# Kernel tuning notes

Hardware: AMD Instinct MI355X
Metric: run time of the kernel (lower is better)

The kernel has to match this reference:

```python
import jax, jax.numpy as jnp
import numpy as np

B, T, HS, H, R = 4, 2048, 1024, 16, 16
D = HS // H  # 64 head_dim
LOGIT_01 = float(np.log(0.1 / 0.9))    # g_proj bias init
LOGIT_098 = float(np.log(0.98 / 0.02)) # base decay logits init


def _rope_cos_sin(seq_len, dim, base=10000.0):
    half = dim // 2
    inv_freq = 1.0 / (base ** (jnp.arange(half, dtype=jnp.float32) / half))
    freqs = jnp.arange(seq_len, dtype=jnp.float32)[:, None] * inv_freq[None, :]  # [T, half]
    return jnp.cos(freqs), jnp.sin(freqs)


def _apply_rope(x, cos, sin):
    # x: [B,T,H,D] with D even; rotate interleaved pairs over full D
    c = cos[None, :, None, :]
    s = sin[None, :, None, :]
    x1 = x[..., 0::2]
    x2 = x[..., 1::2]
    r1 = x1 * c - x2 * s
    r2 = x1 * s + x2 * c
    return jnp.stack((r1, r2), axis=-1).reshape(x.shape)


def setup_inputs() -> dict:
    key = jax.random.key(0)
    ks = jax.random.split(key, 10)
    def rn(k, shape, s=0.02):
        return jax.random.normal(k, shape, dtype=jnp.float32) * s
    return {
        "x": jax.random.normal(ks[0], (B, T, HS), dtype=jnp.float32),
        "q_w": rn(ks[1], (HS, HS)),
        "k_w": rn(ks[2], (HS, HS)),
        "v_w": rn(ks[3], (HS, HS)),
        "Wq": rn(ks[4], (H, R, D), 0.05),
        "Wk": rn(ks[5], (H, R, D), 0.05),
        "g_w": rn(ks[6], (H * R, HS)),
        "g_b": jnp.full((H * R,), LOGIT_01, dtype=jnp.float32),
        "base_decay_logits": jnp.full((H, R), LOGIT_098, dtype=jnp.float32),
        "out_w": rn(ks[7], (HS, HS)),
        "out_b": jnp.zeros((HS,), dtype=jnp.float32),
        "ln_g": jnp.ones((HS,), dtype=jnp.float32),
        "ln_b": jnp.zeros((HS,), dtype=jnp.float32),
    }


def reference(x, q_w, k_w, v_w, Wq, Wk, g_w, g_b, base_decay_logits,
              out_w, out_b, ln_g, ln_b):
    b, t, hs = x.shape
    h, r, d = Wq.shape
    # qkv projections (torch Linear: x @ W.T)
    q = (x @ q_w.T).reshape(b, t, h, d)
    k = (x @ k_w.T).reshape(b, t, h, d)
    v = (x @ v_w.T).reshape(b, t, h, d)
    # RoPE (dim_rot == head_dim since it is even)
    cos, sin = _rope_cos_sin(t, d)
    q = _apply_rope(q, cos, sin)
    k = _apply_rope(k, cos, sin)
    # low-rank projections
    q_r = jnp.einsum('bthd,hrd->bthr', q, Wq)
    k_r = jnp.einsum('bthd,hrd->bthr', k, Wk)
    # content gates
    g = jax.nn.sigmoid((x @ g_w.T + g_b).reshape(b, t, h, r))
    decay = jax.nn.sigmoid(base_decay_logits)[None, :, :, None]  # [1,H,r,1]
    scale = 1.0 / jnp.sqrt(jnp.asarray(d, dtype=x.dtype))

    def step(M, inp):
        q_t, k_t, v_t, g_t = inp  # [B,H,r], [B,H,r], [B,H,D], [B,H,r]
        M = M * decay + jnp.einsum('bhr,bhd->bhrd', g_t * k_t * scale, v_t)
        y = jnp.einsum('bhr,bhrd->bhd', q_t, M)
        return M, y

    xs = (q_r.transpose(1, 0, 2, 3), k_r.transpose(1, 0, 2, 3),
          v.transpose(1, 0, 2, 3), g.transpose(1, 0, 2, 3))
    M0 = jnp.zeros((b, h, r, d), dtype=x.dtype)
    _, Y = jax.lax.scan(step, M0, xs)  # Y: [T,B,H,D]
    Y = Y.transpose(1, 0, 2, 3).reshape(b, t, hs)
    out = Y @ out_w.T + out_b  # dropout is identity at eval time
    hres = x + out
    mu = jnp.mean(hres, axis=-1, keepdims=True)
    var = jnp.mean((hres - mu) ** 2, axis=-1, keepdims=True)
    return (hres - mu) / jnp.sqrt(var + 1e-5) * ln_g + ln_b
```

## Files before the change

kernel.cpp:

```cpp
#include <hip/hip_runtime.h>
#include <hip/hip_bf16.h>

#define B_ 4
#define T_ 2048
#define HS_ 1024
#define H_ 16
#define R_ 16
#define D_ 64
#define BT_ (B_*T_)
#define NC_ 3328
#define CHUNK_ 64
#define NCHUNK_ (T_/CHUNK_)

typedef __attribute__((ext_vector_type(8))) short short8;
typedef __attribute__((ext_vector_type(4))) float f32x4;

__device__ __forceinline__ float b2f(ushort u){
    union{unsigned int i; float f;} v; v.i = ((unsigned int)u) << 16; return v.f;
}
__device__ __forceinline__ ushort f2b(float f){
    __hip_bfloat16 h = __float2bfloat16(f);
    return *reinterpret_cast<ushort*>(&h);
}
__device__ __forceinline__ float sigm(float x){ return 1.f/(1.f+expf(-x)); }

__device__ __forceinline__ void gl_lds16(const void* g, void* l){
    __builtin_amdgcn_global_load_lds((const __attribute__((address_space(1))) void*)g,
                                     (__attribute__((address_space(3))) void*)l,
                                     16, 0, 0);
}

__global__ void k_cast4(const float* __restrict__ src, ushort* __restrict__ dst){
    int i = blockIdx.x*256 + threadIdx.x;
    float4 v = ((const float4*)src)[i];
    ushort4 o; o.x=f2b(v.x); o.y=f2b(v.y); o.z=f2b(v.z); o.w=f2b(v.w);
    ((ushort4*)dst)[i] = o;
}

__global__ void k_build_wcat(const float* __restrict__ qw, const float* __restrict__ kw,
                             const float* __restrict__ vw, const float* __restrict__ gw,
                             ushort* __restrict__ wcat){
    int i = blockIdx.x*256 + threadIdx.x;
    int e = i*4;
    int row = e >> 10, col = e & 1023;
    const float* src;
    if      (row < 1024) src = qw + (size_t)row*1024 + col;
    else if (row < 2048) src = kw + (size_t)(row-1024)*1024 + col;
    else if (row < 3072) src = vw + (size_t)(row-2048)*1024 + col;
    else                 src = gw + (size_t)(row-3072)*1024 + col;
    float4 v = *(const float4*)src;
    ushort4 o; o.x=f2b(v.x); o.y=f2b(v.y); o.z=f2b(v.z); o.w=f2b(v.w);
    ((ushort4*)wcat)[i] = o;
}

__global__ void k_rope_tab(float* __restrict__ cosT, float* __restrict__ sinT){
    int i = blockIdx.x*256 + threadIdx.x;
    int t = i >> 5, f = i & 31;
    float inv = powf(10000.f, -(float)f/32.f);
    float a = (float)t * inv;
    cosT[i] = cosf(a);
    sinT[i] = sinf(a);
}

__global__ __launch_bounds__(256) void k_gemm_bt(const ushort* __restrict__ A,
                                                 const ushort* __restrict__ Bm,
                                                 ushort* __restrict__ C,
                                                 int K, int ldc){
    __shared__ __align__(16) ushort Asl[128*32];
    __shared__ __align__(16) ushort Bsl[128*32];
    int tid  = threadIdx.x;
    int lane = tid & 63, wid = tid >> 6;
    int wrow = (wid >> 1)*64, wcol = (wid & 1)*64;
    long arow0 = (long)blockIdx.x * 128;
    long brow0 = (long)blockIdx.y * 128;

    int srow = tid >> 2, sseg = (tid & 3)*8;
    const ushort* ga0 = A  + (arow0      + srow)*(size_t)K + sseg;
    const ushort* ga1 = ga0 + 64*(size_t)K;
    const ushort* gb0 = Bm + (brow0      + srow)*(size_t)K + sseg;
    const ushort* gb1 = gb0 + 64*(size_t)K;
    ushort* la0 = &Asl[(tid>>6)*512];
    ushort* la1 = la0 + 2048;
    ushort* lb0 = &Bsl[(tid>>6)*512];
    ushort* lb1 = lb0 + 2048;

    f32x4 acc[4][4];
#pragma unroll
    for(int m=0;m<4;m++)
#pragma unroll
        for(int n=0;n<4;n++)
            acc[m][n] = (f32x4){0.f,0.f,0.f,0.f};

    int fr = lane & 15, fg = lane >> 4;
    for(int kt=0; kt<K; kt+=32){
        __syncthreads();
        gl_lds16(ga0 + kt, la0);
        gl_lds16(ga1 + kt, la1);
        gl_lds16(gb0 + kt, lb0);
        gl_lds16(gb1 + kt, lb1);
        __syncthreads();

        short8 af[4], bfr[4];
#pragma unroll
        for(int m=0;m<4;m++) af[m]  = *(const short8*)&Asl[(wrow + m*16 + fr)*32 + fg*8];
#pragma unroll
        for(int n=0;n<4;n++) bfr[n] = *(const short8*)&Bsl[(wcol + n*16 + fr)*32 + fg*8];
#pragma unroll
        for(int m=0;m<4;m++)
#pragma unroll
            for(int n=0;n<4;n++)
                acc[m][n] = __builtin_amdgcn_mfma_f32_16x16x32_bf16(af[m], bfr[n], acc[m][n], 0,0,0);
    }

#pragma unroll
    for(int m=0;m<4;m++)
#pragma unroll
        for(int n=0;n<4;n++){
            long col = brow0 + wcol + n*16 + fr;
#pragma unroll
            for(int j=0;j<4;j++){
                long row = arow0 + wrow + m*16 + fg*4 + j;
                C[row*(long)ldc + col] = f2b(acc[m][n][j]);
            }
        }
}

__global__ __launch_bounds__(256) void k_rope_proj(const ushort* __restrict__ qkvg,
                                                   const float* __restrict__ cosT,
                                                   const float* __restrict__ sinT,
                                                   const float* __restrict__ Wq,
                                                   const float* __restrict__ Wk,
                                                   const float* __restrict__ gb,
                                                   float* __restrict__ qr_s,
                                                   float* __restrict__ gk_s){
    __shared__ __align__(16) ushort lq[64*72], lk[64*72];
    __shared__ __align__(16) ushort wql[16*72], wkl[16*72];
    int tid = threadIdx.x, wid = tid >> 6, lane = tid & 63;
    int bt0 = blockIdx.x * 64;
    int h   = blockIdx.y;

    {
        int row = tid >> 4, seg = tid & 15;
        float4 wq4 = *(const float4*)(Wq + (size_t)h*1024 + row*64 + seg*4);
        float4 wk4 = *(const float4*)(Wk + (size_t)h*1024 + row*64 + seg*4);
        ushort* dq = &wql[row*72 + seg*4];
        ushort* dk = &wkl[row*72 + seg*4];
        dq[0]=f2b(wq4.x); dq[1]=f2b(wq4.y); dq[2]=f2b(wq4.z); dq[3]=f2b(wq4.w);
        dk[0]=f2b(wk4.x); dk[1]=f2b(wk4.y); dk[2]=f2b(wk4.z); dk[3]=f2b(wk4.w);
    }

#pragma unroll
    for(int rep=0; rep<2; ++rep){
        int flat = rep*256 + tid;
        int row = flat >> 3, seg = flat & 7;
        int t = (bt0 + row) & 2047;
        const ushort* base = qkvg + (size_t)(bt0+row)*NC_ + h*64 + seg*8;
        short8 q8 = *(const short8*)base;
        short8 k8 = *(const short8*)(base + 1024);
        float4 cv = *(const float4*)&cosT[t*32 + seg*4];
        float4 sv = *(const float4*)&sinT[t*32 + seg*4];
        float qf[8], kf[8];
#pragma unroll
        for(int j=0;j<8;j++){ qf[j]=b2f((ushort)q8[j]); kf[j]=b2f((ushort)k8[j]); }
        float c4[4] = {cv.x,cv.y,cv.z,cv.w};
        float s4[4] = {sv.x,sv.y,sv.z,sv.w};
        short8 qo, ko;
#pragma unroll
        for(int p=0;p<4;p++){
            float c=c4[p], s=s4[p];
            qo[2*p]   = (short)f2b(qf[2*p]*c - qf[2*p+1]*s);
            qo[2*p+1] = (short)f2b(qf[2*p]*s + qf[2*p+1]*c);
            ko[2*p]   = (short)f2b(kf[2*p]*c - kf[2*p+1]*s);
            ko[2*p+1] = (short)f2b(kf[2*p]*s + kf[2*p+1]*c);
        }
        *(short8*)&lq[row*72 + seg*8] = qo;
        *(short8*)&lk[row*72 + seg*8] = ko;
    }
    __syncthreads();

    int fr = lane & 15, fg = lane >> 4;
    int wrow = wid*16;
    short8 aq0 = *(const short8*)&lq[(wrow+fr)*72 + fg*8];
    short8 aq1 = *(const short8*)&lq[(wrow+fr)*72 + 32 + fg*8];
    short8 ak0 = *(const short8*)&lk[(wrow+fr)*72 + fg*8];
    short8 ak1 = *(const short8*)&lk[(wrow+fr)*72 + 32 + fg*8];
    short8 bq0 = *(const short8*)&wql[fr*72 + fg*8];
    short8 bq1 = *(const short8*)&wql[fr*72 + 32 + fg*8];
    short8 bk0 = *(const short8*)&wkl[fr*72 + fg*8];
    short8 bk1 = *(const short8*)&wkl[fr*72 + 32 + fg*8];
    f32x4 accq = (f32x4){0.f,0.f,0.f,0.f};
    f32x4 acck = (f32x4){0.f,0.f,0.f,0.f};
    accq = __builtin_amdgcn_mfma_f32_16x16x32_bf16(aq0, bq0, accq, 0,0,0);
    accq = __builtin_amdgcn_mfma_f32_16x16x32_bf16(aq1, bq1, accq, 0,0,0);
    acck = __builtin_amdgcn_mfma_f32_16x16x32_bf16(ak0, bk0, acck, 0,0,0);
    acck = __builtin_amdgcn_mfma_f32_16x16x32_bf16(ak1, bk1, acck, 0,0,0);

    int r = fr;
    float gbv = gb[h*16 + r];
#pragma unroll
    for(int j=0;j<4;j++){
        int bt = bt0 + wrow + fg*4 + j;
        int t  = bt & 2047, b = bt >> 11;
        size_t o = (((size_t)(b*16 + h))*2048 + t)*16 + r;
        qr_s[o] = accq[j];
        float gl = b2f(qkvg[(size_t)bt*NC_ + 3072 + h*16 + r]) + gbv;
        gk_s[o] = sigm(gl) * acck[j] * 0.125f;
    }
}

__global__ __launch_bounds__(64) void k_scan_local(const ushort* __restrict__ qkvg,
                                                   const float* __restrict__ gk_s,
                                                   const float* __restrict__ bdl,
                                                   float* __restrict__ Mloc){
    int lane = threadIdx.x;
    int bx = blockIdx.x;
    int ch = bx & (NCHUNK_-1), bh = bx >> 5;
    int b = bh >> 4, h = bh & 15;
    float dec[16], M[16];
#pragma unroll
    for(int r=0;r<16;r++){ dec[r] = sigm(bdl[h*16+r]); M[r] = 0.f; }

    int t0 = ch*CHUNK_;
    const float4*  gk4 = (const float4*)(gk_s + (((size_t)bh)*2048 + t0)*16);
    const ushort*  vp  = qkvg + ((size_t)(b*2048 + t0))*NC_ + 2048 + h*64 + lane;
    for(int tt=0; tt<CHUNK_; ++tt){
        float v = b2f(*vp); vp += NC_;
        float4 a0 = gk4[0], a1 = gk4[1], a2 = gk4[2], a3 = gk4[3]; gk4 += 4;
        float gk[16] = {a0.x,a0.y,a0.z,a0.w, a1.x,a1.y,a1.z,a1.w,
                        a2.x,a2.y,a2.z,a2.w, a3.x,a3.y,a3.z,a3.w};
#pragma unroll
        for(int r=0;r<16;r++) M[r] = fmaf(M[r], dec[r], gk[r]*v);
    }
    float* mp = Mloc + ((size_t)bx)*1024 + lane;
#pragma unroll
    for(int r=0;r<16;r++) mp[r*64] = M[r];
}

__global__ __launch_bounds__(64) void k_scan_carry(float* __restrict__ Mloc,
                                                   const float* __restrict__ bdl){
    int lane = threadIdx.x;
    int sub = blockIdx.x & 3, bh = blockIdx.x >> 2, h = bh & 15;
    float decC[4], S[4];
#pragma unroll
    for(int rr=0;rr<4;rr++){
        decC[rr] = powf(sigm(bdl[h*16 + sub*4 + rr]), (float)CHUNK_);
        S[rr] = 0.f;
    }
    for(int c=0;c<NCHUNK_;c++){
        float* p = Mloc + ((size_t)(bh*NCHUNK_ + c))*1024 + lane + sub*4*64;
#pragma unroll
        for(int rr=0;rr<4;rr++){
            float m = p[rr*64];
            p[rr*64] = S[rr];
            S[rr] = fmaf(S[rr], decC[rr], m);
        }
    }
}

__global__ __launch_bounds__(64) void k_scan_out(const ushort* __restrict__ qkvg,
                                                 const float* __restrict__ gk_s,
                                                 const float* __restrict__ qr_s,
                                                 const float* __restrict__ Mst,
                                                 const float* __restrict__ bdl,
                                                 ushort* __restrict__ Ybf){
    int lane = threadIdx.x;
    int bx = blockIdx.x;
    int ch = bx & (NCHUNK_-1), bh = bx >> 5;
    int b = bh >> 4, h = bh & 15;
    float dec[16], M[16];
#pragma unroll
    for(int r=0;r<16;r++) dec[r] = sigm(bdl[h*16+r]);
    const float* sp = Mst + ((size_t)bx)*1024 + lane;
#pragma unroll
    for(int r=0;r<16;r++) M[r] = sp[r*64];

    int t0 = ch*CHUNK_;
    const float4* gk4 = (const float4*)(gk_s + (((size_t)bh)*2048 + t0)*16);
    const float4* q4  = (const float4*)(qr_s + (((size_t)bh)*2048 + t0)*16);
    const ushort* vp  = qkvg + ((size_t)(b*2048 + t0))*NC_ + 2048 + h*64 + lane;
    ushort*       yp  = Ybf  + ((size_t)(b*2048 + t0))*1024 + h*64 + lane;
    for(int tt=0; tt<CHUNK_; ++tt){
        float v = b2f(*vp); vp += NC_;
        float4 a0 = gk4[0], a1 = gk4[1], a2 = gk4[2], a3 = gk4[3]; gk4 += 4;
        float4 b0 = q4[0],  b1 = q4[1],  b2 = q4[2],  b3 = q4[3];  q4  += 4;
        float gk[16] = {a0.x,a0.y,a0.z,a0.w, a1.x,a1.y,a1.z,a1.w,
                        a2.x,a2.y,a2.z,a2.w, a3.x,a3.y,a3.z,a3.w};
        float qv[16] = {b0.x,b0.y,b0.z,b0.w, b1.x,b1.y,b1.z,b1.w,
                        b2.x,b2.y,b2.z,b2.w, b3.x,b3.y,b3.z,b3.w};
        float y = 0.f;
#pragma unroll
        for(int r=0;r<16;r++){
            M[r] = fmaf(M[r], dec[r], gk[r]*v);
            y    = fmaf(qv[r], M[r], y);
        }
        *yp = f2b(y); yp += 1024;
    }
}

__global__ __launch_bounds__(256) void k_ln(const float* __restrict__ x,
                                            const ushort* __restrict__ O,
                                            const float* __restrict__ ob,
                                            const float* __restrict__ lg,
                                            const float* __restrict__ lb,
                                            float* __restrict__ out){
    __shared__ float red[8];
    int row = blockIdx.x, tid = threadIdx.x;
    float hv[4];
    float sum = 0.f, ssq = 0.f;
#pragma unroll
    for(int k2=0;k2<4;k2++){
        int j = tid + k2*256;
        float v = x[(size_t)row*1024 + j] + b2f(O[(size_t)row*1024 + j]) + ob[j];
        hv[k2] = v; sum += v; ssq += v*v;
    }
#pragma unroll
    for(int off=32; off; off >>= 1){
        sum += __shfl_down(sum, off, 64);
        ssq += __shfl_down(ssq, off, 64);
    }
    int wid = tid >> 6, lane = tid & 63;
    if(lane == 0){ red[wid] = sum; red[4+wid] = ssq; }
    __syncthreads();
    if(tid == 0){
        float s = red[0]+red[1]+red[2]+red[3];
        float q = red[4]+red[5]+red[6]+red[7];
        float mu = s / 1024.f;
        red[0] = mu;
        red[1] = q / 1024.f - mu*mu;
    }
    __syncthreads();
    float mu = red[0];
    float inv = rsqrtf(red[1] + 1e-5f);
#pragma unroll
    for(int k2=0;k2<4;k2++){
        int j = tid + k2*256;
        out[(size_t)row*1024 + j] = (hv[k2]-mu)*inv*lg[j] + lb[j];
    }
}

extern "C" void kernel_launch(void* const* d_in, const int* in_sizes, int n_in,
                              void* d_out, int out_size, void* d_ws, size_t ws_size,
                              hipStream_t stream){
    const float* x    = (const float*)d_in[0];
    const float* q_w  = (const float*)d_in[1];
    const float* k_w  = (const float*)d_in[2];
    const float* v_w  = (const float*)d_in[3];
    const float* Wq   = (const float*)d_in[4];
    const float* Wk   = (const float*)d_in[5];
    const float* g_w  = (const float*)d_in[6];
    const float* g_b  = (const float*)d_in[7];
    const float* bdl  = (const float*)d_in[8];
    const float* outw = (const float*)d_in[9];
    const float* outb = (const float*)d_in[10];
    const float* ln_g = (const float*)d_in[11];
    const float* ln_b = (const float*)d_in[12];
    float* out = (float*)d_out;

    char* ws = (char*)d_ws;
    size_t off = 0;
    ushort* xbf  = (ushort*)(ws + off); off += (size_t)BT_*HS_*2;
    ushort* wcat = (ushort*)(ws + off); off += (size_t)NC_*HS_*2;
    ushort* owbf = (ushort*)(ws + off); off += (size_t)HS_*HS_*2;
    float*  cosT = (float*)(ws + off);  off += (size_t)T_*32*4;
    float*  sinT = (float*)(ws + off);  off += (size_t)T_*32*4;
    ushort* qkvg = (ushort*)(ws + off); off += (size_t)BT_*NC_*2;
    float*  qr_s = (float*)(ws + off);  off += (size_t)BT_*H_*R_*4;
    float*  gk_s = (float*)(ws + off);  off += (size_t)BT_*H_*R_*4;
    float*  Mloc = (float*)(ws + off);  off += (size_t)B_*H_*NCHUNK_*R_*D_*4;
    ushort* Ybf = xbf;
    ushort* O   = qkvg;

    k_cast4<<<(BT_*HS_/4)/256, 256, 0, stream>>>(x, xbf);
    k_build_wcat<<<(NC_*HS_/4)/256, 256, 0, stream>>>(q_w, k_w, v_w, g_w, wcat);
    k_cast4<<<(HS_*HS_/4)/256, 256, 0, stream>>>(outw, owbf);
    k_rope_tab<<<(T_*32)/256, 256, 0, stream>>>(cosT, sinT);

    k_gemm_bt<<<dim3(BT_/128, NC_/128), 256, 0, stream>>>(xbf, wcat, qkvg, HS_, NC_);

    k_rope_proj<<<dim3(BT_/64, H_), 256, 0, stream>>>(qkvg, cosT, sinT, Wq, Wk, g_b, qr_s, gk_s);

    k_scan_local<<<B_*H_*NCHUNK_, 64, 0, stream>>>(qkvg, gk_s, bdl, Mloc);
    k_scan_carry<<<B_*H_*4, 64, 0, stream>>>(Mloc, bdl);
    k_scan_out<<<B_*H_*NCHUNK_, 64, 0, stream>>>(qkvg, gk_s, qr_s, Mloc, bdl, Ybf);

    k_gemm_bt<<<dim3(BT_/128, HS_/128), 256, 0, stream>>>(Ybf, owbf, O, HS_, HS_);

    k_ln<<<BT_, 256, 0, stream>>>(x, O, outb, ln_g, ln_b, out);

    (void)in_sizes; (void)n_in; (void)out_size; (void)ws_size;
}
```

Baseline: 222.4 us.

## Use 256x256-tile double-buffered MFMA GEMM for fused QKVG projection

Adds a new GEMM kernel with 256x256 output tiles, 512 threads, and a K-step of 64. It double-buffers direct global-to-LDS loads with an XOR swizzle, remaps workgroups across the grid, and raises wave priority around the MFMA blocks. It replaces the 128x128 GEMM for the large x·Wcat projection to get more data reuse per tile and to overlap loads with compute. In exchange it uses 128KB of LDS and a large accumulator set, which limits occupancy, and it produces fewer blocks (32x13) to spread across the CUs.

```diff
diff --git a/kernel.cpp b/kernel.cpp
--- a/kernel.cpp
+++ b/kernel.cpp
@@ -60,6 +60,119 @@
     float a = (float)t * inv;
     cosT[i] = cosf(a);
     sinT[i] = sinf(a);
+}
+
+__global__ __launch_bounds__(512, 2) void k_gemm256(const ushort* __restrict__ A,
+                                                    const ushort* __restrict__ Bm,
+                                                    ushort* __restrict__ C,
+                                                    int K, int ldc){
+    __shared__ __align__(16) ushort ldsbuf[65536];
+    const int tid  = threadIdx.x;
+    const int lane = tid & 63, w = tid >> 6;
+    const int fr = lane & 15, fg = lane >> 4;
+    const int wm = w >> 2, wn = w & 3;
+
+    int nwg = gridDim.x * gridDim.y;
+    int lin = blockIdx.y * gridDim.x + blockIdx.x;
+    if((nwg & 7) == 0){
+        int cpx = nwg >> 3;
+        lin = (lin & 7) * cpx + (lin >> 3);
+    }
+    const int bx = lin % gridDim.x, by = lin / gridDim.x;
+    const long arow0 = (long)bx * 256;
+    const long brow0 = (long)by * 256;
+
+    const ushort* gsrcA[4];
+    const ushort* gsrcB[4];
+#pragma unroll
+    for(int l=0;l<4;l++){
+        int p = l*8192 + w*1024 + lane*16;
+        int q = p ^ (((p>>9)&1)<<5);
+        int row = q >> 7, col = (q & 127) >> 1;
+        gsrcA[l] = A  + (arow0 + row)*(size_t)K + col;
+        gsrcB[l] = Bm + (brow0 + row)*(size_t)K + col;
+    }
+
+#define STAGE256(t, buf) do{                                                   \
+    ushort* _b = &ldsbuf[(buf)*32768 + w*512];                                 \
+    _Pragma("unroll")                                                          \
+    for(int l=0;l<4;l++) gl_lds16(gsrcA[l] + (t)*64, _b + l*4096);             \
+    _Pragma("unroll")                                                          \
+    for(int l=0;l<4;l++) gl_lds16(gsrcB[l] + (t)*64, _b + 16384 + l*4096);     \
+}while(0)
+
+    f32x4 acc[8][4];
+#pragma unroll
+    for(int m=0;m<8;m++)
+#pragma unroll
+        for(int n=0;n<4;n++)
+            acc[m][n] = (f32x4){0.f,0.f,0.f,0.f};
+
+    const int NT = K >> 6;
+    STAGE256(0, 0);
+    STAGE256(1, 1);
+
+    for(int t=0; t<NT; ++t){
+        const int cur = t & 1;
+        if(t < NT-1) asm volatile("s_waitcnt vmcnt(8)" ::: "memory");
+        else         asm volatile("s_waitcnt vmcnt(0)" ::: "memory");
+        __builtin_amdgcn_s_barrier();
+        __builtin_amdgcn_sched_barrier(0);
+
+        const ushort* Areg = &ldsbuf[cur*32768];
+        const ushort* Breg = &ldsbuf[cur*32768 + 16384];
+
+#pragma unroll
+        for(int mh=0; mh<2; ++mh)
+#pragma unroll
+        for(int nh=0; nh<2; ++nh){
+            short8 af[4][2], bv[2][2];
+#pragma unroll
+            for(int mm=0; mm<4; ++mm)
+#pragma unroll
+            for(int ks=0; ks<2; ++ks){
+                int p = ((wm*128 + (mh*4+mm)*16 + fr) << 7) + ((ks*4+fg) << 4);
+                p ^= ((p>>9)&1) << 5;
+                af[mm][ks] = *(const short8*)((const char*)Areg + p);
+            }
+#pragma unroll
+            for(int nn=0; nn<2; ++nn)
+#pragma unroll
+            for(int ks=0; ks<2; ++ks){
+                int p = ((wn*64 + (nh*2+nn)*16 + fr) << 7) + ((ks*4+fg) << 4);
+                p ^= ((p>>9)&1) << 5;
+                bv[nn][ks] = *(const short8*)((const char*)Breg + p);
+            }
+            __builtin_amdgcn_s_setprio(1);
+#pragma unroll
+            for(int mm=0; mm<4; ++mm)
+#pragma unroll
+            for(int nn=0; nn<2; ++nn)
+#pragma unroll
+            for(int ks=0; ks<2; ++ks)
+                acc[mh*4+mm][nh*2+nn] = __builtin_amdgcn_mfma_f32_16x16x32_bf16(
+                    af[mm][ks], bv[nn][ks], acc[mh*4+mm][nh*2+nn], 0,0,0);
+            __builtin_amdgcn_s_setprio(0);
+            __builtin_amdgcn_sched_barrier(0);
+        }
+
+        __builtin_amdgcn_s_barrier();
+        __builtin_amdgcn_sched_barrier(0);
+        if(t+2 < NT) STAGE256(t+2, cur);
+    }
+#undef STAGE256
+
+#pragma unroll
+    for(int m=0;m<8;m++)
+#pragma unroll
+        for(int n=0;n<4;n++){
+            long col = brow0 + wn*64 + n*16 + fr;
+#pragma unroll
+            for(int j=0;j<4;j++){
+                long row = arow0 + wm*128 + m*16 + fg*4 + j;
+                C[row*(size_t)ldc + col] = f2b(acc[m][n][j]);
+            }
+        }
 }
 
 __global__ __launch_bounds__(256) void k_gemm_bt(const ushort* __restrict__ A,
@@ -375,7 +488,7 @@
     k_cast4<<<(HS_*HS_/4)/256, 256, 0, stream>>>(outw, owbf);
     k_rope_tab<<<(T_*32)/256, 256, 0, stream>>>(cosT, sinT);
 
-    k_gemm_bt<<<dim3(BT_/128, NC_/128), 256, 0, stream>>>(xbf, wcat, qkvg, HS_, NC_);
+    k_gemm256<<<dim3(BT_/256, NC_/256), 512, 0, stream>>>(xbf, wcat, qkvg, HS_, NC_);
 
     k_rope_proj<<<dim3(BT_/64, H_), 256, 0, stream>>>(qkvg, cosT, sinT, Wq, Wk, g_b, qr_s, gk_s);
 
```

Result: no change. 222.7 us (+0.1%).

## Replace GEMM with double-buffered 256x128 tile kernel using XCD-aware block swizzle

Applied to the files above, without the earlier changes.

The bf16 MFMA GEMM now uses 512-thread blocks computing 256x128 tiles. The LDS buffer is double-buffered so the next K-slice loads while the current one is multiplied, cutting the two barriers per iteration down to one. It also adds a rotated LDS column layout to reduce bank conflicts, remaps block IDs so neighbouring tiles share an XCD's L2, and raises wave priority around the MFMA block. The risks are higher register and LDS use per block, fewer blocks in the grid for the smaller output GEMM, and dependence on the swizzle matching how blocks are dispatched.

```diff
diff --git a/kernel.cpp b/kernel.cpp
--- a/kernel.cpp
+++ b/kernel.cpp
@@ -62,27 +62,39 @@
     sinT[i] = sinf(a);
 }
 
-__global__ __launch_bounds__(256) void k_gemm_bt(const ushort* __restrict__ A,
-                                                 const ushort* __restrict__ Bm,
-                                                 ushort* __restrict__ C,
-                                                 int K, int ldc){
-    __shared__ __align__(16) ushort Asl[128*32];
-    __shared__ __align__(16) ushort Bsl[128*32];
-    int tid  = threadIdx.x;
-    int lane = tid & 63, wid = tid >> 6;
-    int wrow = (wid >> 1)*64, wcol = (wid & 1)*64;
-    long arow0 = (long)blockIdx.x * 128;
-    long brow0 = (long)blockIdx.y * 128;
-
-    int srow = tid >> 2, sseg = (tid & 3)*8;
-    const ushort* ga0 = A  + (arow0      + srow)*(size_t)K + sseg;
-    const ushort* ga1 = ga0 + 64*(size_t)K;
-    const ushort* gb0 = Bm + (brow0      + srow)*(size_t)K + sseg;
-    const ushort* gb1 = gb0 + 64*(size_t)K;
-    ushort* la0 = &Asl[(tid>>6)*512];
-    ushort* la1 = la0 + 2048;
-    ushort* lb0 = &Bsl[(tid>>6)*512];
-    ushort* lb1 = lb0 + 2048;
+__global__ __launch_bounds__(512, 4) void k_gemm256d(const ushort* __restrict__ A,
+                                                     const ushort* __restrict__ Bm,
+                                                     ushort* __restrict__ C,
+                                                     int K, int ldc){
+    __shared__ __align__(16) ushort lds[24576];
+    const int tid  = threadIdx.x;
+    const int lane = tid & 63, w = tid >> 6;
+    const int fr = lane & 15, fg = lane >> 4;
+    const int wm = w >> 1, wn = w & 1;
+    const int qa = ((fg + fr) & 3) * 8;
+
+    int mt = gridDim.x;
+    int L = blockIdx.y * mt + blockIdx.x;
+    int bxi, byi;
+    int msub = mt >> 3;
+    if((mt & 7) == 0 && msub > 0){
+        int xcd = L & 7, c = L >> 3;
+        bxi = xcd * msub + (c % msub);
+        byi = c / msub;
+    } else { bxi = blockIdx.x; byi = blockIdx.y; }
+    const long arow0 = (long)bxi * 256;
+    const long brow0 = (long)byi * 128;
+
+    const int srow = tid >> 2;
+    const int scol = ((((tid & 3) - (tid >> 2)) & 3)) * 8;
+    const ushort* gsrc0 = A  + (arow0 +       srow) * (size_t)K + scol;
+    const ushort* gsrc1 = A  + (arow0 + 128 + srow) * (size_t)K + scol;
+    const ushort* gsrc2 = Bm + (brow0 +       srow) * (size_t)K + scol;
+
+#define STG(t) do{ ushort* _b = &lds[((t)&1)*12288 + w*512];                  \
+    gl_lds16(gsrc0 + (size_t)(t)*32, _b);                                     \
+    gl_lds16(gsrc1 + (size_t)(t)*32, _b + 4096);                              \
+    gl_lds16(gsrc2 + (size_t)(t)*32, _b + 8192); }while(0)
 
     f32x4 acc[4][4];
 #pragma unroll
@@ -91,36 +103,41 @@
         for(int n=0;n<4;n++)
             acc[m][n] = (f32x4){0.f,0.f,0.f,0.f};
 
-    int fr = lane & 15, fg = lane >> 4;
-    for(int kt=0; kt<K; kt+=32){
-        __syncthreads();
-        gl_lds16(ga0 + kt, la0);
-        gl_lds16(ga1 + kt, la1);
-        gl_lds16(gb0 + kt, lb0);
-        gl_lds16(gb1 + kt, lb1);
-        __syncthreads();
-
-        short8 af[4], bfr[4];
-#pragma unroll
-        for(int m=0;m<4;m++) af[m]  = *(const short8*)&Asl[(wrow + m*16 + fr)*32 + fg*8];
-#pragma unroll
-        for(int n=0;n<4;n++) bfr[n] = *(const short8*)&Bsl[(wcol + n*16 + fr)*32 + fg*8];
-#pragma unroll
-        for(int m=0;m<4;m++)
-#pragma unroll
-            for(int n=0;n<4;n++)
-                acc[m][n] = __builtin_amdgcn_mfma_f32_16x16x32_bf16(af[m], bfr[n], acc[m][n], 0,0,0);
-    }
+    const int NT = K >> 5;
+    STG(0);
+    for(int t=0; t<NT; ++t){
+        asm volatile("s_waitcnt vmcnt(0)" ::: "memory");
+        __builtin_amdgcn_s_barrier();
+        __builtin_amdgcn_sched_barrier(0);
+        if(t+1 < NT) STG(t+1);
+        const int sb = (t&1)*12288;
+        short8 af[4], bv[4];
+#pragma unroll
+        for(int mm=0; mm<4; ++mm)
+            af[mm] = *(const short8*)&lds[sb + (wm*64 + mm*16 + fr)*32 + qa];
+#pragma unroll
+        for(int nf=0; nf<4; ++nf)
+            bv[nf] = *(const short8*)&lds[sb + 8192 + (wn*64 + nf*16 + fr)*32 + qa];
+        __builtin_amdgcn_s_setprio(1);
+#pragma unroll
+        for(int mm=0; mm<4; ++mm)
+#pragma unroll
+        for(int nf=0; nf<4; ++nf)
+            acc[mm][nf] = __builtin_amdgcn_mfma_f32_16x16x32_bf16(
+                af[mm], bv[nf], acc[mm][nf], 0,0,0);
+        __builtin_amdgcn_s_setprio(0);
+    }
+#undef STG
 
 #pragma unroll
     for(int m=0;m<4;m++)
 #pragma unroll
         for(int n=0;n<4;n++){
-            long col = brow0 + wcol + n*16 + fr;
+            long col = brow0 + wn*64 + n*16 + fr;
 #pragma unroll
             for(int j=0;j<4;j++){
-                long row = arow0 + wrow + m*16 + fg*4 + j;
-                C[row*(long)ldc + col] = f2b(acc[m][n][j]);
+                long row = arow0 + wm*64 + m*16 + fg*4 + j;
+                C[row*(size_t)ldc + col] = f2b(acc[m][n][j]);
             }
         }
 }
@@ -375,7 +392,7 @@
     k_cast4<<<(HS_*HS_/4)/256, 256, 0, stream>>>(outw, owbf);
     k_rope_tab<<<(T_*32)/256, 256, 0, stream>>>(cosT, sinT);
 
-    k_gemm_bt<<<dim3(BT_/128, NC_/128), 256, 0, stream>>>(xbf, wcat, qkvg, HS_, NC_);
+    k_gemm256d<<<dim3(BT_/256, NC_/128), 512, 0, stream>>>(xbf, wcat, qkvg, HS_, NC_);
 
     k_rope_proj<<<dim3(BT_/64, H_), 256, 0, stream>>>(qkvg, cosT, sinT, Wq, Wk, g_b, qr_s, gk_s);
 
@@ -383,7 +400,7 @@
     k_scan_carry<<<B_*H_*4, 64, 0, stream>>>(Mloc, bdl);
     k_scan_out<<<B_*H_*NCHUNK_, 64, 0, stream>>>(qkvg, gk_s, qr_s, Mloc, bdl, Ybf);
 
-    k_gemm_bt<<<dim3(BT_/128, HS_/128), 256, 0, stream>>>(Ybf, owbf, O, HS_, HS_);
+    k_gemm256d<<<dim3(BT_/256, HS_/128), 512, 0, stream>>>(Ybf, owbf, O, HS_, HS_);
 
     k_ln<<<BT_, 256, 0, stream>>>(x, O, outb, ln_g, ln_b, out);
 
```

After: 199.7 us. -10.2%, faster.
